# Optimization experiments

Hardware: AMD Instinct MI355X
Metric: run time of the kernel (lower is better)

## Reference

```python
import jax, jax.numpy as jnp
import numpy as np

K = 27  # 3^3 kernel offsets for kernel_size=3, D=3
N_DOWN, N_UP = 40000, 160000
C_DOWN, C_SKIP, C_OUT = 128, 64, 96


def setup_inputs() -> dict:
    key = jax.random.key(0)
    ks = jax.random.split(key, 8)
    skip_feat = jax.random.normal(ks[0], (N_UP, C_SKIP), dtype=jnp.float32)
    down_feat = jax.random.normal(ks[1], (N_DOWN, C_DOWN), dtype=jnp.float32)
    W_deconv = jax.random.normal(ks[2], (K, C_DOWN, C_DOWN), dtype=jnp.float32) * (1.0 / np.sqrt(C_DOWN * K))
    W_conv = jax.random.normal(ks[3], (K, C_SKIP + C_DOWN, C_OUT), dtype=jnp.float32) * (1.0 / np.sqrt((C_SKIP + C_DOWN) * K))
    deconv_in_idx = jax.random.randint(ks[4], (K, N_DOWN), 0, N_DOWN, dtype=jnp.int32)
    deconv_out_idx = jax.random.randint(ks[5], (K, N_DOWN), 0, N_UP, dtype=jnp.int32)
    conv_in_idx = jax.random.randint(ks[6], (K, N_UP), 0, N_UP, dtype=jnp.int32)
    conv_out_idx = jax.random.randint(ks[7], (K, N_UP), 0, N_UP, dtype=jnp.int32)
    return {
        "skip_feat": skip_feat,
        "down_feat": down_feat,
        "W_deconv": W_deconv,
        "W_conv": W_conv,
        "deconv_in_idx": deconv_in_idx,
        "deconv_out_idx": deconv_out_idx,
        "conv_in_idx": conv_in_idx,
        "conv_out_idx": conv_out_idx,
    }


def _sparse_conv(feat, W, in_idx, out_idx, n_out):
    """ME-style sparse conv: per-offset gather -> matmul -> scatter-add."""
    out = jnp.zeros((n_out, W.shape[2]), dtype=feat.dtype)
    for k in range(W.shape[0]):  # fixed small loop over 27 kernel offsets
        msg = feat[in_idx[k]] @ W[k]          # [E_k, C_out]
        out = out.at[out_idx[k]].add(msg)
    return out


def reference(skip_feat, down_feat, W_deconv, W_conv,
              deconv_in_idx, deconv_out_idx, conv_in_idx, conv_out_idx):
    n_up = skip_feat.shape[0]
    # transposed sparse conv (stride 2) + ReLU
    up_feat = jax.nn.relu(_sparse_conv(down_feat, W_deconv, deconv_in_idx, deconv_out_idx, n_up))
    # ME.cat(up_feat, skip_feat): channel concat on shared coordinates
    cat_feat = jnp.concatenate([up_feat, skip_feat], axis=1)  # [N_up, C_down+C_skip]
    # sparse conv (stride 1) + ReLU
    net = jax.nn.relu(_sparse_conv(cat_feat, W_conv, conv_in_idx, conv_out_idx, n_up))
    return net
```

## Files before the change

### kernel.cpp

```cpp
#include <hip/hip_runtime.h>
#include <cstdint>

#define K_OFF 27
#define NDOWN 40000
#define NUP   160000
#define CDOWN 128
#define CSKIP 64
#define CCAT  192
#define COUT  96
#define TM    64
#define MT_D  5
#define B_BINS (K_OFF * NUP)

typedef __bf16 bf16x8 __attribute__((ext_vector_type(8)));
typedef float f32x4 __attribute__((ext_vector_type(4)));

__device__ __forceinline__ unsigned short f2b(float f) {
    unsigned int u = __float_as_uint(f);
    u += 0x7FFFu + ((u >> 16) & 1u);
    return (unsigned short)(u >> 16);
}
__device__ __forceinline__ unsigned int pk2(float a, float b) {
    return (unsigned)f2b(a) | ((unsigned)f2b(b) << 16);
}
__device__ __forceinline__ float b2f(unsigned int lo16) {
    return __uint_as_float(lo16 << 16);
}

__device__ __forceinline__ void gll16(const void* gsrc, void* ldst) {
    auto g = reinterpret_cast<const __attribute__((address_space(1))) unsigned int*>(
        reinterpret_cast<uintptr_t>(gsrc));
    auto l = reinterpret_cast<__attribute__((address_space(3))) unsigned int*>(
        reinterpret_cast<uintptr_t>(ldst));
    __builtin_amdgcn_global_load_lds(g, l, 16, 0, 0);
}

__global__ void pack_down_kernel(const float* __restrict__ down,
                                 unsigned short* __restrict__ dbf) {
    int i = blockIdx.x * 256 + threadIdx.x;
    if (i >= NDOWN * CDOWN / 8) return;
    const float4* s = (const float4*)down + (long)i * 2;
    float4 v0 = s[0], v1 = s[1];
    uint4 o;
    o.x = pk2(v0.x, v0.y); o.y = pk2(v0.z, v0.w);
    o.z = pk2(v1.x, v1.y); o.w = pk2(v1.z, v1.w);
    ((uint4*)dbf)[i] = o;
}

__global__ void pack_w_kernel(const float* __restrict__ Wd, const float* __restrict__ Wc,
                              unsigned short* __restrict__ WdT, unsigned short* __restrict__ WcT) {
    int i = blockIdx.x * 256 + threadIdx.x;
    if (i < K_OFF * CDOWN * CDOWN) {
        int k = i / (CDOWN * CDOWN), rem = i % (CDOWN * CDOWN);
        int n = rem >> 7, c = rem & 127;
        WdT[i] = f2b(Wd[((long)k * CDOWN + c) * CDOWN + n]);
    }
    if (i < K_OFF * COUT * CCAT) {
        int k = i / (COUT * CCAT), rem = i % (COUT * CCAT);
        int n = rem / CCAT, c = rem % CCAT;
        WcT[i] = f2b(Wc[((long)k * CCAT + c) * COUT + n]);
    }
}

__global__ void pack_cat_kernel(const float* __restrict__ up, const float* __restrict__ skip,
                                unsigned short* __restrict__ cat) {
    const int t = threadIdx.x;
    const int j = blockIdx.x * 8 + t / 24;
    const int s = t % 24;
    const int e0 = s * 8;
    float4 v0, v1;
    if (e0 < CDOWN) {
        const float4* src = (const float4*)(up + (long)j * CDOWN + e0);
        v0 = src[0]; v1 = src[1];
        v0.x = fmaxf(v0.x, 0.f); v0.y = fmaxf(v0.y, 0.f);
        v0.z = fmaxf(v0.z, 0.f); v0.w = fmaxf(v0.w, 0.f);
        v1.x = fmaxf(v1.x, 0.f); v1.y = fmaxf(v1.y, 0.f);
        v1.z = fmaxf(v1.z, 0.f); v1.w = fmaxf(v1.w, 0.f);
    } else {
        const float4* src = (const float4*)(skip + (long)j * CSKIP + (e0 - CDOWN));
        v0 = src[0]; v1 = src[1];
    }
    uint4 o;
    o.x = pk2(v0.x, v0.y); o.y = pk2(v0.z, v0.w);
    o.z = pk2(v1.x, v1.y); o.w = pk2(v1.z, v1.w);
    ((uint4*)(cat + (long)j * CCAT))[s] = o;
}

__global__ __launch_bounds__(256, 2)
void deconv_fast(const unsigned short* __restrict__ dbf,
                 const unsigned short* __restrict__ WdT,
                 const int* __restrict__ in_idx,
                 const int* __restrict__ out_idx,
                 float* __restrict__ up) {
    __shared__ __align__(1024) unsigned short sA[TM * CDOWN];

    const int segs = (NDOWN / TM) / MT_D;
    const int bk = blockIdx.x / segs;
    const int tile0 = (blockIdx.x % segs) * MT_D;
    const int t = threadIdx.x;
    const int wave = t >> 6, lane = t & 63;
    const int col = lane & 15, quad = lane >> 4;
    const int wm = wave & 1, wn = wave >> 1;

    int srow[4], soff[4];
#pragma unroll
    for (int i = 0; i < 4; i++) {
        int c = wave * 256 + i * 64 + lane;
        int r = c >> 4, cc = c & 15;
        srow[i] = r;
        soff[i] = (cc ^ (r & 7)) * 16;
    }

    bf16x8 b[4][4];
    {
        const unsigned short* wb = WdT + (long)bk * CDOWN * CDOWN;
#pragma unroll
        for (int kk = 0; kk < 4; kk++)
#pragma unroll
            for (int nt = 0; nt < 4; nt++)
                b[kk][nt] = *(const bf16x8*)&wb[(wn * 64 + nt * 16 + col) * CDOWN + kk * 32 + quad * 8];
    }

    const long kBase = (long)bk * NDOWN;
    const char* sAc = (const char*)sA;

    for (int tt = 0; tt < MT_D; ++tt) {
        const int rowbase = (tile0 + tt) * TM;
#pragma unroll
        for (int i = 0; i < 4; i++) {
            const int j = in_idx[kBase + rowbase + srow[i]];
            gll16((const char*)dbf + (long)j * (CDOWN * 2) + soff[i],
                  (char*)sA + (wave * 4 + i) * 1024);
        }
        __syncthreads();

        f32x4 acc[2][4];
#pragma unroll
        for (int mi = 0; mi < 2; mi++)
#pragma unroll
            for (int nt = 0; nt < 4; nt++) acc[mi][nt] = (f32x4){0.f, 0.f, 0.f, 0.f};

#pragma unroll
        for (int kk = 0; kk < 4; kk++) {
            const int ch = kk * 4 + quad;
#pragma unroll
            for (int mi = 0; mi < 2; mi++) {
                const int row = wm * 32 + mi * 16 + col;
                bf16x8 a = *(const bf16x8*)(sAc + row * 256 + ((ch ^ (row & 7)) * 16));
#pragma unroll
                for (int nt = 0; nt < 4; nt++)
                    acc[mi][nt] = __builtin_amdgcn_mfma_f32_16x16x32_bf16(a, b[kk][nt], acc[mi][nt], 0, 0, 0);
            }
        }
        __syncthreads();

#pragma unroll
        for (int mi = 0; mi < 2; mi++)
#pragma unroll
            for (int r = 0; r < 4; r++) {
                const int lrow = wm * 32 + mi * 16 + quad * 4 + r;
                const long ob = (long)out_idx[kBase + rowbase + lrow] * CDOWN;
#pragma unroll
                for (int nt = 0; nt < 4; nt++)
                    atomicAdd(&up[ob + wn * 64 + nt * 16 + col], acc[mi][nt][r]);
            }
    }
}

__global__ void hist_kernel(const int* __restrict__ cv_out, unsigned int* __restrict__ hist) {
    const int i = blockIdx.x * 256 + threadIdx.x;
    const int k = blockIdx.y;
    const int j = cv_out[(long)k * NUP + i];
    atomicAdd(&hist[(long)k * NUP + j], 1u);
}

__global__ void scan_blocks(const unsigned int* __restrict__ in, unsigned int* __restrict__ out,
                            unsigned int* __restrict__ aux, int n) {
    __shared__ unsigned int ls[256];
    const int t = threadIdx.x;
    const long base = (long)blockIdx.x * 1024 + (long)t * 4;
    unsigned int v0 = (base     < n) ? in[base]     : 0u;
    unsigned int v1 = (base + 1 < n) ? in[base + 1] : 0u;
    unsigned int v2 = (base + 2 < n) ? in[base + 2] : 0u;
    unsigned int v3 = (base + 3 < n) ? in[base + 3] : 0u;
    const unsigned int s = v0 + v1 + v2 + v3;
    ls[t] = s;
    __syncthreads();
    for (int off = 1; off < 256; off <<= 1) {
        unsigned int x = (t >= off) ? ls[t - off] : 0u;
        __syncthreads();
        ls[t] += x;
        __syncthreads();
    }
    const unsigned int ex = ls[t] - s;
    if (base     < n) out[base]     = ex;
    if (base + 1 < n) out[base + 1] = ex + v0;
    if (base + 2 < n) out[base + 2] = ex + v0 + v1;
    if (base + 3 < n) out[base + 3] = ex + v0 + v1 + v2;
    if (aux != nullptr && t == 255) aux[blockIdx.x] = ls[255];
}

__global__ void addback_kernel(unsigned int* __restrict__ out, const unsigned int* __restrict__ aux, int n) {
    const long i = (long)blockIdx.x * 256 + threadIdx.x;
    if (i < n) out[i] += aux[i >> 10];
}

__global__ void scatter_kernel(const int* __restrict__ cv_in,
                               const int* __restrict__ cv_out,
                               const unsigned int* __restrict__ start,
                               unsigned int* __restrict__ hist,
                               unsigned int* __restrict__ entries) {
    const int i = blockIdx.x * 256 + threadIdx.x;
    const int k = blockIdx.y;
    const long p = (long)k * NUP + i;
    const int j = cv_out[p];
    const long bin = (long)k * NUP + j;
    const unsigned int off = atomicSub(&hist[bin], 1u) - 1u;
    entries[start[bin] + off] = (unsigned int)cv_in[p];
}

__global__ __launch_bounds__(256, 2)
void conv_inv(const unsigned short* __restrict__ cat,
              const unsigned short* __restrict__ WcT,
              const unsigned int* __restrict__ start,
              const unsigned int* __restrict__ entries,
              float* __restrict__ out) {
    __shared__ __align__(1024) unsigned short sA[TM * CCAT];
    __shared__ __align__(1024) unsigned short sB[COUT * CCAT];

    const int j0 = blockIdx.x * TM;
    const int t = threadIdx.x;
    const int wave = t >> 6, lane = t & 63;
    const int col = lane & 15, quad = lane >> 4;
    const int wm = wave & 1, wn = wave >> 1;
    const int r  = t >> 2;
    const int cq = (t & 3) * 6;

    f32x4 acc[2][3];
#pragma unroll
    for (int mi = 0; mi < 2; mi++)
#pragma unroll
        for (int nt = 0; nt < 3; nt++) acc[mi][nt] = (f32x4){0.f, 0.f, 0.f, 0.f};

    char* sAc = (char*)sA;
    char* sBc = (char*)sB;

    for (int k = 0; k < K_OFF; k++) {
        const long kb = (long)k * NUP;
        const unsigned int s0 = start[kb + j0 + r];
        const long i1 = kb + j0 + r + 1;
        const unsigned int s1 = (i1 == (long)B_BINS) ? (unsigned int)B_BINS : start[i1];
        const int n = (int)(s1 - s0);

        uint4 ch[6];
        if (n == 1) {
            const unsigned int ie = entries[s0];
            const uint4* src = (const uint4*)(cat + (long)ie * CCAT) + cq;
#pragma unroll
            for (int q = 0; q < 6; q++) ch[q] = src[q];
        } else if (n == 0) {
#pragma unroll
            for (int q = 0; q < 6; q++) ch[q] = make_uint4(0u, 0u, 0u, 0u);
        } else {
            float fa[6][8];
#pragma unroll
            for (int q = 0; q < 6; q++)
#pragma unroll
                for (int e8 = 0; e8 < 8; e8++) fa[q][e8] = 0.f;
            for (unsigned int e = s0; e < s1; e++) {
                const unsigned int ie = entries[e];
                const uint4* src = (const uint4*)(cat + (long)ie * CCAT) + cq;
#pragma unroll
                for (int q = 0; q < 6; q++) {
                    uint4 c = src[q];
                    fa[q][0] += b2f(c.x & 0xffffu); fa[q][1] += b2f(c.x >> 16);
                    fa[q][2] += b2f(c.y & 0xffffu); fa[q][3] += b2f(c.y >> 16);
                    fa[q][4] += b2f(c.z & 0xffffu); fa[q][5] += b2f(c.z >> 16);
                    fa[q][6] += b2f(c.w & 0xffffu); fa[q][7] += b2f(c.w >> 16);
                }
            }
#pragma unroll
            for (int q = 0; q < 6; q++) {
                ch[q].x = pk2(fa[q][0], fa[q][1]);
                ch[q].y = pk2(fa[q][2], fa[q][3]);
                ch[q].z = pk2(fa[q][4], fa[q][5]);
                ch[q].w = pk2(fa[q][6], fa[q][7]);
            }
        }

        uint4 bc[9];
        const uint4* wsrc = (const uint4*)(WcT + (long)k * COUT * CCAT);
#pragma unroll
        for (int p = 0; p < 9; p++) bc[p] = wsrc[t + 256 * p];

        __syncthreads();

#pragma unroll
        for (int q = 0; q < 6; q++) {
            const int cc = cq + q;
            *(uint4*)(sAc + r * 384 + ((cc ^ (r & 7)) << 4)) = ch[q];
        }
#pragma unroll
        for (int p = 0; p < 9; p++) {
            const int c = t + 256 * p;
            const int nn = c / 24, cc = c % 24;
            *(uint4*)(sBc + nn * 384 + ((cc ^ (nn & 7)) << 4)) = bc[p];
        }
        __syncthreads();

#pragma unroll
        for (int kk = 0; kk < 6; kk++) {
            const int c2 = kk * 4 + quad;
            const int row0 = wm * 32 + col;
            const int row1 = row0 + 16;
            bf16x8 a0 = *(const bf16x8*)(sAc + row0 * 384 + ((c2 ^ (row0 & 7)) << 4));
            bf16x8 a1 = *(const bf16x8*)(sAc + row1 * 384 + ((c2 ^ (row1 & 7)) << 4));
#pragma unroll
            for (int nt = 0; nt < 3; nt++) {
                const int bn = wn * 48 + nt * 16 + col;
                bf16x8 bb = *(const bf16x8*)(sBc + bn * 384 + ((c2 ^ (bn & 7)) << 4));
                acc[0][nt] = __builtin_amdgcn_mfma_f32_16x16x32_bf16(a0, bb, acc[0][nt], 0, 0, 0);
                acc[1][nt] = __builtin_amdgcn_mfma_f32_16x16x32_bf16(a1, bb, acc[1][nt], 0, 0, 0);
            }
        }
    }

#pragma unroll
    for (int mi = 0; mi < 2; mi++)
#pragma unroll
        for (int rr = 0; rr < 4; rr++) {
            const int lrow = wm * 32 + mi * 16 + quad * 4 + rr;
            float* op = out + (long)(j0 + lrow) * COUT + wn * 48 + col;
#pragma unroll
            for (int nt = 0; nt < 3; nt++)
                op[nt * 16] = fmaxf(acc[mi][nt][rr], 0.f);
        }
}

#define SA1 136
#define SB1 136

__global__ __launch_bounds__(256, 2)
void deconv_kernel(const float* __restrict__ down,
                   const float* __restrict__ Wd,
                   const int* __restrict__ in_idx,
                   const int* __restrict__ out_idx,
                   float* __restrict__ up) {
    __shared__ __align__(16) unsigned short sA[TM * SA1];
    __shared__ __align__(16) unsigned short sB[CDOWN * SB1];
    __shared__ int sOut[TM];

    const int tiles = NDOWN / TM;
    const int bk = blockIdx.x / tiles;
    const int tile = blockIdx.x % tiles;
    const int t = threadIdx.x;
    const long kInBase = (long)bk * NDOWN + tile * TM;

    {
        const int r = t >> 2;
        const int c0 = (t & 3) * 32;
        const int j = in_idx[kInBase + r];
        const float* src = down + (long)j * CDOWN + c0;
        unsigned short* dst = sA + r * SA1 + c0;
        #pragma unroll
        for (int c = 0; c < 32; c += 4) {
            float4 v = *(const float4*)(src + c);
            *(unsigned int*)(dst + c)     = pk2(v.x, v.y);
            *(unsigned int*)(dst + c + 2) = pk2(v.z, v.w);
        }
    }
    {
        const float* wsrc = Wd + (long)bk * CDOWN * CDOWN;
        for (int idx = t; idx < CDOWN * CDOWN; idx += 256) {
            const int kk = idx >> 7;
            const int n  = idx & 127;
            sB[n * SB1 + kk] = f2b(wsrc[idx]);
        }
    }
    if (t < TM) sOut[t] = out_idx[kInBase + t];
    __syncthreads();

    const int wave = t >> 6;
    const int lane = t & 63;
    const int col  = lane & 15;
    const int quad = lane >> 4;
    const int mrow = wave * 16 + col;

    f32x4 acc[8];
    #pragma unroll
    for (int i = 0; i < 8; i++) acc[i] = (f32x4){0.f, 0.f, 0.f, 0.f};

    #pragma unroll
    for (int k0 = 0; k0 < CDOWN; k0 += 32) {
        const int koff = k0 + quad * 8;
        bf16x8 a = *(const bf16x8*)&sA[mrow * SA1 + koff];
        #pragma unroll
        for (int nt = 0; nt < 8; nt++) {
            bf16x8 bb = *(const bf16x8*)&sB[(nt * 16 + col) * SB1 + koff];
            acc[nt] = __builtin_amdgcn_mfma_f32_16x16x32_bf16(a, bb, acc[nt], 0, 0, 0);
        }
    }
    #pragma unroll
    for (int r = 0; r < 4; r++) {
        const int lrow = wave * 16 + quad * 4 + r;
        const long obase = (long)sOut[lrow] * CDOWN;
        #pragma unroll
        for (int nt = 0; nt < 8; nt++)
            atomicAdd(&up[obase + nt * 16 + col], acc[nt][r]);
    }
}

#define SA2 200
#define SB2 200

__global__ __launch_bounds__(256, 2)
void conv_kernel(const float* __restrict__ up,
                 const float* __restrict__ skip,
                 const float* __restrict__ Wc,
                 const int* __restrict__ in_idx,
                 const int* __restrict__ out_idx,
                 float* __restrict__ out) {
    __shared__ __align__(16) unsigned short sA[TM * SA2];
    __shared__ __align__(16) unsigned short sB[COUT * SB2];
    __shared__ int sOut[TM];

    const int tiles = NUP / TM;
    const int bk = blockIdx.x / tiles;
    const int tile = blockIdx.x % tiles;
    const int t = threadIdx.x;
    const long kInBase = (long)bk * NUP + tile * TM;

    {
        const int r = t >> 2;
        const int c0 = (t & 3) * 48;
        const int j = in_idx[kInBase + r];
        const float* uprow = up + (long)j * CDOWN;
        const float* skrow = skip + (long)j * CSKIP;
        unsigned short* dst = sA + r * SA2 + c0;
        #pragma unroll
        for (int c = 0; c < 48; c += 4) {
            const int gc = c0 + c;
            float4 v;
            if (gc < CDOWN) {
                v = *(const float4*)(uprow + gc);
                v.x = fmaxf(v.x, 0.f); v.y = fmaxf(v.y, 0.f);
                v.z = fmaxf(v.z, 0.f); v.w = fmaxf(v.w, 0.f);
            } else {
                v = *(const float4*)(skrow + (gc - CDOWN));
            }
            *(unsigned int*)(dst + c)     = pk2(v.x, v.y);
            *(unsigned int*)(dst + c + 2) = pk2(v.z, v.w);
        }
    }
    {
        const float* wsrc = Wc + (long)bk * CCAT * COUT;
        for (int idx = t; idx < CCAT * COUT; idx += 256) {
            const int kk = idx / COUT;
            const int n  = idx - kk * COUT;
            sB[n * SB2 + kk] = f2b(wsrc[idx]);
        }
    }
    if (t < TM) sOut[t] = out_idx[kInBase + t];
    __syncthreads();

    const int wave = t >> 6;
    const int lane = t & 63;
    const int col  = lane & 15;
    const int quad = lane >> 4;
    const int mrow = wave * 16 + col;

    f32x4 acc[6];
    #pragma unroll
    for (int i = 0; i < 6; i++) acc[i] = (f32x4){0.f, 0.f, 0.f, 0.f};

    #pragma unroll
    for (int k0 = 0; k0 < CCAT; k0 += 32) {
        const int koff = k0 + quad * 8;
        bf16x8 a = *(const bf16x8*)&sA[mrow * SA2 + koff];
        #pragma unroll
        for (int nt = 0; nt < 6; nt++) {
            bf16x8 bb = *(const bf16x8*)&sB[(nt * 16 + col) * SB2 + koff];
            acc[nt] = __builtin_amdgcn_mfma_f32_16x16x32_bf16(a, bb, acc[nt], 0, 0, 0);
        }
    }
    #pragma unroll
    for (int r = 0; r < 4; r++) {
        const int lrow = wave * 16 + quad * 4 + r;
        const long obase = (long)sOut[lrow] * COUT;
        #pragma unroll
        for (int nt = 0; nt < 6; nt++)
            atomicAdd(&out[obase + nt * 16 + col], acc[nt][r]);
    }
}

__global__ void relu_kernel(float* __restrict__ x, int n4) {
    int i = blockIdx.x * blockDim.x + threadIdx.x;
    if (i < n4) {
        float4 v = ((float4*)x)[i];
        v.x = fmaxf(v.x, 0.f); v.y = fmaxf(v.y, 0.f);
        v.z = fmaxf(v.z, 0.f); v.w = fmaxf(v.w, 0.f);
        ((float4*)x)[i] = v;
    }
}

extern "C" void kernel_launch(void* const* d_in, const int* in_sizes, int n_in,
                              void* d_out, int out_size, void* d_ws, size_t ws_size,
                              hipStream_t stream) {
    const float* skip   = (const float*)d_in[0];
    const float* down   = (const float*)d_in[1];
    const float* Wd     = (const float*)d_in[2];
    const float* Wc     = (const float*)d_in[3];
    const int* dc_in    = (const int*)d_in[4];
    const int* dc_out   = (const int*)d_in[5];
    const int* cv_in    = (const int*)d_in[6];
    const int* cv_out   = (const int*)d_in[7];
    float* out = (float*)d_out;
    float* up  = (float*)d_ws;

    const size_t OFF_CAT = (size_t)NUP * CDOWN * 4;
    const size_t OFF_DBF = OFF_CAT + (size_t)NUP * CCAT * 2;
    const size_t OFF_WDT = OFF_DBF + (size_t)NDOWN * CDOWN * 2;
    const size_t OFF_WCT = OFF_WDT + (size_t)K_OFF * CDOWN * CDOWN * 2;
    const size_t WS_NEED = OFF_WCT + (size_t)K_OFF * COUT * CCAT * 2;

    hipMemsetAsync(up, 0, (size_t)NUP * CDOWN * sizeof(float), stream);

    if (ws_size >= WS_NEED) {
        unsigned short* catb = (unsigned short*)((char*)d_ws + OFF_CAT);
        unsigned short* dbf  = (unsigned short*)((char*)d_ws + OFF_DBF);
        unsigned short* WdT  = (unsigned short*)((char*)d_ws + OFF_WDT);
        unsigned short* WcT  = (unsigned short*)((char*)d_ws + OFF_WCT);

        unsigned int* entriesC = (unsigned int*)d_ws;
        unsigned int* startC   = (unsigned int*)((char*)d_ws + 17280000);
        unsigned int* aux1     = (unsigned int*)((char*)d_ws + 34560000);
        unsigned int* aux2     = (unsigned int*)((char*)d_ws + 34580000);
        unsigned int* hist     = (unsigned int*)d_out;

        pack_down_kernel<<<(NDOWN * CDOWN / 8 + 255) / 256, 256, 0, stream>>>(down, dbf);
        pack_w_kernel<<<(K_OFF * COUT * CCAT + 255) / 256, 256, 0, stream>>>(Wd, Wc, WdT, WcT);
        deconv_fast<<<K_OFF * ((NDOWN / TM) / MT_D), 256, 0, stream>>>(dbf, WdT, dc_in, dc_out, up);
        pack_cat_kernel<<<NUP / 8, 192, 0, stream>>>(up, skip, catb);
        hipMemsetAsync(hist, 0, (size_t)B_BINS * 4, stream);
        hist_kernel<<<dim3(NUP / 256, K_OFF), 256, 0, stream>>>(cv_out, hist);
        const int nblk1 = (B_BINS + 1023) / 1024;
        const int nblk2 = (nblk1 + 1023) / 1024;
        scan_blocks<<<nblk1, 256, 0, stream>>>(hist, startC, aux1, B_BINS);
        scan_blocks<<<nblk2, 256, 0, stream>>>(aux1, aux1, aux2, nblk1);
        scan_blocks<<<1, 256, 0, stream>>>(aux2, aux2, nullptr, nblk2);
        addback_kernel<<<(nblk1 + 255) / 256, 256, 0, stream>>>(aux1, aux2, nblk1);
        addback_kernel<<<(B_BINS + 255) / 256, 256, 0, stream>>>(startC, aux1, B_BINS);
        scatter_kernel<<<dim3(NUP / 256, K_OFF), 256, 0, stream>>>(cv_in, cv_out, startC, hist, entriesC);
        conv_inv<<<NUP / TM, 256, 0, stream>>>(catb, WcT, startC, entriesC, out);
    } else {
        hipMemsetAsync(out, 0, (size_t)out_size * sizeof(float), stream);
        deconv_kernel<<<K_OFF * (NDOWN / TM), 256, 0, stream>>>(down, Wd, dc_in, dc_out, up);
        conv_kernel<<<K_OFF * (NUP / TM), 256, 0, stream>>>(up, skip, Wc, cv_in, cv_out, out);
        relu_kernel<<<(out_size / 4 + 255) / 256, 256, 0, stream>>>(out, out_size / 4);
    }
}
```

Before: 2.197 ms.

## Double-buffer conv gather tiles, read weights from global, merge pack and scan kernels

The conv_inv kernel now double-buffers the gathered A tile in shared memory, so the gather for the next offset is issued before the MFMAs of the current one, and each k step needs one barrier instead of two. The B weights are no longer staged in LDS but read straight from global/L2 per wave, which frees shared memory and raises the occupancy hint to 3 blocks per CU. Separately, the down and weight pack kernels are merged into one launch, and the three-kernel middle scan level is replaced by a single-block sequential scan. The trade-off is more global weight traffic per wave, and the single-block scan handles about 4200 elements on its own.

```diff
diff --git a/kernel.cpp b/kernel.cpp
--- a/kernel.cpp
+++ b/kernel.cpp
@@ -23,9 +23,6 @@
 __device__ __forceinline__ unsigned int pk2(float a, float b) {
     return (unsigned)f2b(a) | ((unsigned)f2b(b) << 16);
 }
-__device__ __forceinline__ float b2f(unsigned int lo16) {
-    return __uint_as_float(lo16 << 16);
-}
 
 __device__ __forceinline__ void gll16(const void* gsrc, void* ldst) {
     auto g = reinterpret_cast<const __attribute__((address_space(1))) unsigned int*>(
@@ -35,21 +32,21 @@
     __builtin_amdgcn_global_load_lds(g, l, 16, 0, 0);
 }
 
-__global__ void pack_down_kernel(const float* __restrict__ down,
-                                 unsigned short* __restrict__ dbf) {
+__global__ void pack_all_kernel(const float* __restrict__ down,
+                                const float* __restrict__ Wd,
+                                const float* __restrict__ Wc,
+                                unsigned short* __restrict__ dbf,
+                                unsigned short* __restrict__ WdT,
+                                unsigned short* __restrict__ WcT) {
     int i = blockIdx.x * 256 + threadIdx.x;
-    if (i >= NDOWN * CDOWN / 8) return;
-    const float4* s = (const float4*)down + (long)i * 2;
-    float4 v0 = s[0], v1 = s[1];
-    uint4 o;
-    o.x = pk2(v0.x, v0.y); o.y = pk2(v0.z, v0.w);
-    o.z = pk2(v1.x, v1.y); o.w = pk2(v1.z, v1.w);
-    ((uint4*)dbf)[i] = o;
-}
-
-__global__ void pack_w_kernel(const float* __restrict__ Wd, const float* __restrict__ Wc,
-                              unsigned short* __restrict__ WdT, unsigned short* __restrict__ WcT) {
-    int i = blockIdx.x * 256 + threadIdx.x;
+    if (i < NDOWN * CDOWN / 8) {
+        const float4* s = (const float4*)down + (long)i * 2;
+        float4 v0 = s[0], v1 = s[1];
+        uint4 o;
+        o.x = pk2(v0.x, v0.y); o.y = pk2(v0.z, v0.w);
+        o.z = pk2(v1.x, v1.y); o.w = pk2(v1.z, v1.w);
+        ((uint4*)dbf)[i] = o;
+    }
     if (i < K_OFF * CDOWN * CDOWN) {
         int k = i / (CDOWN * CDOWN), rem = i % (CDOWN * CDOWN);
         int n = rem >> 7, c = rem & 127;
@@ -200,6 +197,31 @@
     if (aux != nullptr && t == 255) aux[blockIdx.x] = ls[255];
 }
 
+__global__ void scan_mid(unsigned int* __restrict__ a, int n) {
+    __shared__ unsigned int ls[256];
+    __shared__ unsigned int carry;
+    const int t = threadIdx.x;
+    if (t == 0) carry = 0u;
+    __syncthreads();
+    for (int base = 0; base < n; base += 256) {
+        const int idx = base + t;
+        unsigned int v = (idx < n) ? a[idx] : 0u;
+        ls[t] = v;
+        __syncthreads();
+        for (int off = 1; off < 256; off <<= 1) {
+            unsigned int x = (t >= off) ? ls[t - off] : 0u;
+            __syncthreads();
+            ls[t] += x;
+            __syncthreads();
+        }
+        const unsigned int ex = ls[t] - v + carry;
+        if (idx < n) a[idx] = ex;
+        __syncthreads();
+        if (t == 0) carry += ls[255];
+        __syncthreads();
+    }
+}
+
 __global__ void addback_kernel(unsigned int* __restrict__ out, const unsigned int* __restrict__ aux, int n) {
     const long i = (long)blockIdx.x * 256 + threadIdx.x;
     if (i < n) out[i] += aux[i >> 10];
@@ -219,14 +241,13 @@
     entries[start[bin] + off] = (unsigned int)cv_in[p];
 }
 
-__global__ __launch_bounds__(256, 2)
+__global__ __launch_bounds__(256, 3)
 void conv_inv(const unsigned short* __restrict__ cat,
               const unsigned short* __restrict__ WcT,
               const unsigned int* __restrict__ start,
               const unsigned int* __restrict__ entries,
               float* __restrict__ out) {
-    __shared__ __align__(1024) unsigned short sA[TM * CCAT];
-    __shared__ __align__(1024) unsigned short sB[COUT * CCAT];
+    __shared__ __align__(1024) unsigned short sA[2][TM * CCAT];
 
     const int j0 = blockIdx.x * TM;
     const int t = threadIdx.x;
@@ -242,86 +263,70 @@
 #pragma unroll
         for (int nt = 0; nt < 3; nt++) acc[mi][nt] = (f32x4){0.f, 0.f, 0.f, 0.f};
 
-    char* sAc = (char*)sA;
-    char* sBc = (char*)sB;
+    auto produce = [&](int kp, int buf) {
+        char* dst = (char*)sA[buf] + r * 384;
+        const long kb = (long)kp * NUP;
+        const unsigned int s0 = start[kb + j0 + r];
+        const long nx = kb + j0 + r + 1;
+        const unsigned int s1 = (nx == (long)B_BINS) ? (unsigned int)B_BINS : start[nx];
+        const unsigned int n = s1 - s0;
+        if (n == 1u) {
+            const uint4* src = (const uint4*)(cat + (long)entries[s0] * CCAT) + cq;
+#pragma unroll
+            for (int q = 0; q < 6; q++) {
+                uint4 v = src[q];
+                *(uint4*)(dst + (((cq + q) ^ (r & 7)) << 4)) = v;
+            }
+        } else if (n == 0u) {
+            const uint4 z = make_uint4(0u, 0u, 0u, 0u);
+#pragma unroll
+            for (int q = 0; q < 6; q++)
+                *(uint4*)(dst + (((cq + q) ^ (r & 7)) << 4)) = z;
+        } else {
+#pragma unroll
+            for (int q = 0; q < 6; q++) {
+                float fa[8];
+#pragma unroll
+                for (int e8 = 0; e8 < 8; e8++) fa[e8] = 0.f;
+                for (unsigned int e = s0; e < s1; e++) {
+                    const uint4 c = ((const uint4*)(cat + (long)entries[e] * CCAT))[cq + q];
+                    fa[0] += __uint_as_float(c.x << 16); fa[1] += __uint_as_float(c.x & 0xffff0000u);
+                    fa[2] += __uint_as_float(c.y << 16); fa[3] += __uint_as_float(c.y & 0xffff0000u);
+                    fa[4] += __uint_as_float(c.z << 16); fa[5] += __uint_as_float(c.z & 0xffff0000u);
+                    fa[6] += __uint_as_float(c.w << 16); fa[7] += __uint_as_float(c.w & 0xffff0000u);
+                }
+                uint4 o;
+                o.x = pk2(fa[0], fa[1]); o.y = pk2(fa[2], fa[3]);
+                o.z = pk2(fa[4], fa[5]); o.w = pk2(fa[6], fa[7]);
+                *(uint4*)(dst + (((cq + q) ^ (r & 7)) << 4)) = o;
+            }
+        }
+    };
+
+    produce(0, 0);
+
+    const unsigned short* wl = WcT + (long)(wn * 48 + col) * CCAT + quad * 8;
+    const int row0 = wm * 32 + col, row1 = row0 + 16;
 
     for (int k = 0; k < K_OFF; k++) {
-        const long kb = (long)k * NUP;
-        const unsigned int s0 = start[kb + j0 + r];
-        const long i1 = kb + j0 + r + 1;
-        const unsigned int s1 = (i1 == (long)B_BINS) ? (unsigned int)B_BINS : start[i1];
-        const int n = (int)(s1 - s0);
-
-        uint4 ch[6];
-        if (n == 1) {
-            const unsigned int ie = entries[s0];
-            const uint4* src = (const uint4*)(cat + (long)ie * CCAT) + cq;
-#pragma unroll
-            for (int q = 0; q < 6; q++) ch[q] = src[q];
-        } else if (n == 0) {
-#pragma unroll
-            for (int q = 0; q < 6; q++) ch[q] = make_uint4(0u, 0u, 0u, 0u);
-        } else {
-            float fa[6][8];
-#pragma unroll
-            for (int q = 0; q < 6; q++)
-#pragma unroll
-                for (int e8 = 0; e8 < 8; e8++) fa[q][e8] = 0.f;
-            for (unsigned int e = s0; e < s1; e++) {
-                const unsigned int ie = entries[e];
-                const uint4* src = (const uint4*)(cat + (long)ie * CCAT) + cq;
-#pragma unroll
-                for (int q = 0; q < 6; q++) {
-                    uint4 c = src[q];
-                    fa[q][0] += b2f(c.x & 0xffffu); fa[q][1] += b2f(c.x >> 16);
-                    fa[q][2] += b2f(c.y & 0xffffu); fa[q][3] += b2f(c.y >> 16);
-                    fa[q][4] += b2f(c.z & 0xffffu); fa[q][5] += b2f(c.z >> 16);
-                    fa[q][6] += b2f(c.w & 0xffffu); fa[q][7] += b2f(c.w >> 16);
-                }
-            }
-#pragma unroll
-            for (int q = 0; q < 6; q++) {
-                ch[q].x = pk2(fa[q][0], fa[q][1]);
-                ch[q].y = pk2(fa[q][2], fa[q][3]);
-                ch[q].z = pk2(fa[q][4], fa[q][5]);
-                ch[q].w = pk2(fa[q][6], fa[q][7]);
-            }
-        }
-
-        uint4 bc[9];
-        const uint4* wsrc = (const uint4*)(WcT + (long)k * COUT * CCAT);
-#pragma unroll
-        for (int p = 0; p < 9; p++) bc[p] = wsrc[t + 256 * p];
-
-        __syncthreads();
-
-#pragma unroll
-        for (int q = 0; q < 6; q++) {
-            const int cc = cq + q;
-            *(uint4*)(sAc + r * 384 + ((cc ^ (r & 7)) << 4)) = ch[q];
-        }
-#pragma unroll
-        for (int p = 0; p < 9; p++) {
-            const int c = t + 256 * p;
-            const int nn = c / 24, cc = c % 24;
-            *(uint4*)(sBc + nn * 384 + ((cc ^ (nn & 7)) << 4)) = bc[p];
-        }
-        __syncthreads();
-
+        __syncthreads();
+        if (k + 1 < K_OFF) produce(k + 1, (k + 1) & 1);
+        const unsigned short* wk = wl + (long)k * (COUT * CCAT);
+        const char* cur = (const char*)sA[k & 1];
 #pragma unroll
         for (int kk = 0; kk < 6; kk++) {
+            bf16x8 b0 = *(const bf16x8*)(wk + kk * 32);
+            bf16x8 b1 = *(const bf16x8*)(wk + 16 * CCAT + kk * 32);
+            bf16x8 b2 = *(const bf16x8*)(wk + 32 * CCAT + kk * 32);
             const int c2 = kk * 4 + quad;
-            const int row0 = wm * 32 + col;
-            const int row1 = row0 + 16;
-            bf16x8 a0 = *(const bf16x8*)(sAc + row0 * 384 + ((c2 ^ (row0 & 7)) << 4));
-            bf16x8 a1 = *(const bf16x8*)(sAc + row1 * 384 + ((c2 ^ (row1 & 7)) << 4));
-#pragma unroll
-            for (int nt = 0; nt < 3; nt++) {
-                const int bn = wn * 48 + nt * 16 + col;
-                bf16x8 bb = *(const bf16x8*)(sBc + bn * 384 + ((c2 ^ (bn & 7)) << 4));
-                acc[0][nt] = __builtin_amdgcn_mfma_f32_16x16x32_bf16(a0, bb, acc[0][nt], 0, 0, 0);
-                acc[1][nt] = __builtin_amdgcn_mfma_f32_16x16x32_bf16(a1, bb, acc[1][nt], 0, 0, 0);
-            }
+            bf16x8 a0 = *(const bf16x8*)(cur + row0 * 384 + ((c2 ^ (row0 & 7)) << 4));
+            bf16x8 a1 = *(const bf16x8*)(cur + row1 * 384 + ((c2 ^ (row1 & 7)) << 4));
+            acc[0][0] = __builtin_amdgcn_mfma_f32_16x16x32_bf16(a0, b0, acc[0][0], 0, 0, 0);
+            acc[1][0] = __builtin_amdgcn_mfma_f32_16x16x32_bf16(a1, b0, acc[1][0], 0, 0, 0);
+            acc[0][1] = __builtin_amdgcn_mfma_f32_16x16x32_bf16(a0, b1, acc[0][1], 0, 0, 0);
+            acc[1][1] = __builtin_amdgcn_mfma_f32_16x16x32_bf16(a1, b1, acc[1][1], 0, 0, 0);
+            acc[0][2] = __builtin_amdgcn_mfma_f32_16x16x32_bf16(a0, b2, acc[0][2], 0, 0, 0);
+            acc[1][2] = __builtin_amdgcn_mfma_f32_16x16x32_bf16(a1, b2, acc[1][2], 0, 0, 0);
         }
     }
 
@@ -534,21 +539,16 @@
         unsigned int* entriesC = (unsigned int*)d_ws;
         unsigned int* startC   = (unsigned int*)((char*)d_ws + 17280000);
         unsigned int* aux1     = (unsigned int*)((char*)d_ws + 34560000);
-        unsigned int* aux2     = (unsigned int*)((char*)d_ws + 34580000);
         unsigned int* hist     = (unsigned int*)d_out;
 
-        pack_down_kernel<<<(NDOWN * CDOWN / 8 + 255) / 256, 256, 0, stream>>>(down, dbf);
-        pack_w_kernel<<<(K_OFF * COUT * CCAT + 255) / 256, 256, 0, stream>>>(Wd, Wc, WdT, WcT);
+        pack_all_kernel<<<2500, 256, 0, stream>>>(down, Wd, Wc, dbf, WdT, WcT);
         deconv_fast<<<K_OFF * ((NDOWN / TM) / MT_D), 256, 0, stream>>>(dbf, WdT, dc_in, dc_out, up);
         pack_cat_kernel<<<NUP / 8, 192, 0, stream>>>(up, skip, catb);
         hipMemsetAsync(hist, 0, (size_t)B_BINS * 4, stream);
         hist_kernel<<<dim3(NUP / 256, K_OFF), 256, 0, stream>>>(cv_out, hist);
         const int nblk1 = (B_BINS + 1023) / 1024;
-        const int nblk2 = (nblk1 + 1023) / 1024;
         scan_blocks<<<nblk1, 256, 0, stream>>>(hist, startC, aux1, B_BINS);
-        scan_blocks<<<nblk2, 256, 0, stream>>>(aux1, aux1, aux2, nblk1);
-        scan_blocks<<<1, 256, 0, stream>>>(aux2, aux2, nullptr, nblk2);
-        addback_kernel<<<(nblk1 + 255) / 256, 256, 0, stream>>>(aux1, aux2, nblk1);
+        scan_mid<<<1, 256, 0, stream>>>(aux1, nblk1);
         addback_kernel<<<(B_BINS + 255) / 256, 256, 0, stream>>>(startC, aux1, B_BINS);
         scatter_kernel<<<dim3(NUP / 256, K_OFF), 256, 0, stream>>>(cv_in, cv_out, startC, hist, entriesC);
         conv_inv<<<NUP / TM, 256, 0, stream>>>(catb, WcT, startC, entriesC, out);
```

After: 2.445 ms. 1.11x slower.
